# Kernel optimization log

Measured on AMD Instinct MI355X. Metric: run time of the kernel, lower is better.

The kernel has to match this reference:

```python
import jax, jax.numpy as jnp
import numpy as np
import math

H = 768
NH = 12
D = H // NH


def setup_inputs() -> dict:
    key = jax.random.key(0)
    ks = jax.random.split(key, 13)
    B, S = 1, 384
    s = 0.02
    inp = {
        "hidden_states": jax.random.normal(ks[0], (B, S, H), jnp.float32),
        "attention_mask": jnp.zeros((B, 1, 1, S), jnp.float32),
        "pos_emb": jax.random.normal(ks[1], (B, S, S, H), jnp.float32),
        "Wq": jax.random.normal(ks[2], (H, H), jnp.float32) * s,
        "bq": jnp.zeros((H,), jnp.float32),
        "Wk": jax.random.normal(ks[3], (H, H), jnp.float32) * s,
        "bk": jnp.zeros((H,), jnp.float32),
        "Wv": jax.random.normal(ks[4], (H, H), jnp.float32) * s,
        "bv": jnp.zeros((H,), jnp.float32),
        "Wpk": jax.random.normal(ks[5], (H, H), jnp.float32) * s,
        "bpk": jnp.zeros((H,), jnp.float32),
        "Wpq": jax.random.normal(ks[6], (H, H), jnp.float32) * s,
        "bpq": jnp.zeros((H,), jnp.float32),
    }
    return inp


def reference(hidden_states, attention_mask, pos_emb,
              Wq, bq, Wk, bk, Wv, bv, Wpk, bpk, Wpq, bpq):
    B, S, Hd = hidden_states.shape
    split = lambda x: x.reshape(B, S, NH, D).transpose(0, 2, 1, 3)  # -> (B, h, S, d)
    q = split(hidden_states @ Wq + bq)
    k = split(hidden_states @ Wk + bk)
    v = split(hidden_states @ Wv + bv)

    # content-to-content
    c2c = jnp.einsum('bhid,bhjd->bhij', q, k)

    # per-pair position projections: (B,S,S,H) -> (B,S,S,h,d)
    pos_key = (pos_emb @ Wpk + bpk).reshape(B, S, S, NH, D)
    pos_query = (pos_emb @ Wpq + bpq).reshape(B, S, S, NH, D)

    # content-to-position: q[b,h,i,:] . pos_key[b,i,j,h,:]
    c2p = jnp.einsum('bhid,bijhd->bhij', q, pos_key)
    # position-to-content: pos_query[b,j,i,h,:] . k[b,h,j,:]
    p2c = jnp.einsum('bjihd,bhjd->bhij', pos_query, k)

    scores = (c2c + c2p + p2c) / math.sqrt(D) + attention_mask
    probs = jax.nn.softmax(scores, axis=-1)  # dropout is identity (p=0 / eval)
    ctx = jnp.einsum('bhij,bhjd->bhid', probs, v)
    return ctx.transpose(0, 2, 1, 3).reshape(B, S, Hd)
```

## Files before the change

### kernel.cpp

```cpp
#include <hip/hip_runtime.h>
#include <math.h>

#define SEQ 384
#define HDIM 768
#define NHEAD 12
#define DHEAD 64

__global__ __launch_bounds__(256)
void qkv_gemm(const float* __restrict__ X,
              const float* __restrict__ Wq, const float* __restrict__ bq,
              const float* __restrict__ Wk, const float* __restrict__ bk,
              const float* __restrict__ Wv, const float* __restrict__ bv,
              float* __restrict__ q, float* __restrict__ k, float* __restrict__ v)
{
    __shared__ float Xs[16][68];
    __shared__ float Ws[16][68];
    const int z = blockIdx.z;
    const float* W    = (z == 0) ? Wq : (z == 1) ? Wk : Wv;
    const float* bias = (z == 0) ? bq : (z == 1) ? bk : bv;
    float* out        = (z == 0) ? q  : (z == 1) ? k  : v;

    const int m0 = blockIdx.x * 64;
    const int n0 = blockIdx.y * 64;
    const int tid = threadIdx.x;
    const int ty = tid / 16, tx = tid % 16;

    const int lxm = tid / 4,  lxk = (tid % 4) * 4;
    const int lwk = tid / 16, lwn = (tid % 16) * 4;

    float acc[4][4] = {};

    for (int k0 = 0; k0 < HDIM; k0 += 16) {
        float4 xa = *(const float4*)&X[(m0 + lxm) * HDIM + k0 + lxk];
        float4 wa = *(const float4*)&W[(size_t)(k0 + lwk) * HDIM + n0 + lwn];
        __syncthreads();
        Xs[lxk + 0][lxm] = xa.x; Xs[lxk + 1][lxm] = xa.y;
        Xs[lxk + 2][lxm] = xa.z; Xs[lxk + 3][lxm] = xa.w;
        *(float4*)&Ws[lwk][lwn] = wa;
        __syncthreads();
        #pragma unroll
        for (int kk = 0; kk < 16; kk++) {
            float4 a4 = *(const float4*)&Xs[kk][4 * ty];
            float4 b4 = *(const float4*)&Ws[kk][4 * tx];
            float a[4] = {a4.x, a4.y, a4.z, a4.w};
            float b[4] = {b4.x, b4.y, b4.z, b4.w};
            #pragma unroll
            for (int ia = 0; ia < 4; ia++)
                #pragma unroll
                for (int ib = 0; ib < 4; ib++)
                    acc[ia][ib] = fmaf(a[ia], b[ib], acc[ia][ib]);
        }
    }
    float4 bv4 = *(const float4*)&bias[n0 + 4 * tx];
    #pragma unroll
    for (int ia = 0; ia < 4; ia++) {
        float4 o;
        o.x = acc[ia][0] + bv4.x; o.y = acc[ia][1] + bv4.y;
        o.z = acc[ia][2] + bv4.z; o.w = acc[ia][3] + bv4.w;
        *(float4*)&out[(size_t)(m0 + 4 * ty + ia) * HDIM + n0 + 4 * tx] = o;
    }
}

__global__ __launch_bounds__(256)
void pos_proj(const float* __restrict__ q, const float* __restrict__ k,
              const float* __restrict__ Wpk, const float* __restrict__ Wpq,
              float* __restrict__ qp, float* __restrict__ kp)
{
    __shared__ float As[64][68];
    __shared__ float Bs[64][68];
    const int h = blockIdx.z % NHEAD;
    const int s = blockIdx.z / NHEAD;
    const float* Asrc = s ? k   : q;
    const float* Wsrc = s ? Wpq : Wpk;
    float* out        = s ? kp  : qp;

    const int i0 = blockIdx.x * 64, e0 = blockIdx.y * 64;
    const int tid = threadIdx.x;
    const int dg = tid % 16, row = tid / 16;

    #pragma unroll
    for (int r = 0; r < 4; r++) {
        const int rr = r * 16 + row;
        float4 a4 = *(const float4*)&Asrc[(size_t)(i0 + rr) * HDIM + h * 64 + dg * 4];
        float4 b4 = *(const float4*)&Wsrc[(size_t)(e0 + rr) * HDIM + h * 64 + dg * 4];
        As[dg * 4 + 0][rr - 0] = a4.x; As[dg * 4 + 1][rr] = a4.y;
        As[dg * 4 + 2][rr] = a4.z;     As[dg * 4 + 3][rr] = a4.w;
        Bs[dg * 4 + 0][rr] = b4.x;     Bs[dg * 4 + 1][rr] = b4.y;
        Bs[dg * 4 + 2][rr] = b4.z;     Bs[dg * 4 + 3][rr] = b4.w;
    }
    __syncthreads();

    const int ty = tid / 16, tx = tid % 16;
    float acc[4][4] = {};
    #pragma unroll 4
    for (int d = 0; d < 64; d++) {
        float4 a4 = *(const float4*)&As[d][4 * ty];
        float4 b4 = *(const float4*)&Bs[d][4 * tx];
        float a[4] = {a4.x, a4.y, a4.z, a4.w};
        float b[4] = {b4.x, b4.y, b4.z, b4.w};
        #pragma unroll
        for (int ia = 0; ia < 4; ia++)
            #pragma unroll
            for (int ib = 0; ib < 4; ib++)
                acc[ia][ib] = fmaf(a[ia], b[ib], acc[ia][ib]);
    }
    #pragma unroll
    for (int ia = 0; ia < 4; ia++) {
        float4 o = make_float4(acc[ia][0], acc[ia][1], acc[ia][2], acc[ia][3]);
        *(float4*)&out[((size_t)(i0 + 4 * ty + ia) * NHEAD + h) * HDIM + e0 + 4 * tx] = o;
    }
}

__global__ __launch_bounds__(192)
void scores_pos(const float* __restrict__ pe, const float* __restrict__ qp,
                const float* __restrict__ kp,
                float* __restrict__ A1, float* __restrict__ P2T)
{
    __shared__ float Ps[32][388];
    __shared__ float Ws[32][24];
    const int i  = blockIdx.x;
    const int tid = threadIdx.x;
    const int rg = tid / 96;
    const int jl = tid % 96;

    const float* pebase = pe + (size_t)i * SEQ * HDIM;
    const int wr  = tid / 8;
    const int wec = tid % 8;
    const float* wsrc = (wr < NHEAD)
        ? (qp + ((size_t)i * NHEAD + wr) * HDIM)
        : (kp + ((size_t)i * NHEAD + (wr - NHEAD)) * HDIM);

    float acc[12][4] = {};

    for (int c = 0; c < 24; c++) {
        const int e0 = c * 32;
        __syncthreads();
        float4 w4 = *(const float4*)&wsrc[e0 + wec * 4];
        Ws[wec * 4 + 0][wr] = w4.x; Ws[wec * 4 + 1][wr] = w4.y;
        Ws[wec * 4 + 2][wr] = w4.z; Ws[wec * 4 + 3][wr] = w4.w;
        #pragma unroll
        for (int rnd = 0; rnd < 16; rnd++) {
            const int jrow = rnd * 24 + wr;
            float4 p4 = *(const float4*)&pebase[(size_t)jrow * HDIM + e0 + wec * 4];
            Ps[wec * 4 + 0][jrow] = p4.x; Ps[wec * 4 + 1][jrow] = p4.y;
            Ps[wec * 4 + 2][jrow] = p4.z; Ps[wec * 4 + 3][jrow] = p4.w;
        }
        __syncthreads();
        #pragma unroll 2
        for (int ee = 0; ee < 32; ee++) {
            float4 p4 = *(const float4*)&Ps[ee][4 * jl];
            float4 wa = *(const float4*)&Ws[ee][12 * rg + 0];
            float4 wb = *(const float4*)&Ws[ee][12 * rg + 4];
            float4 wc = *(const float4*)&Ws[ee][12 * rg + 8];
            float p[4] = {p4.x, p4.y, p4.z, p4.w};
            float w[12] = {wa.x, wa.y, wa.z, wa.w, wb.x, wb.y, wb.z, wb.w,
                           wc.x, wc.y, wc.z, wc.w};
            #pragma unroll
            for (int r = 0; r < 12; r++)
                #pragma unroll
                for (int u = 0; u < 4; u++)
                    acc[r][u] = fmaf(w[r], p[u], acc[r][u]);
        }
    }
    float* dst = (rg == 0) ? A1 : P2T;
    #pragma unroll
    for (int r = 0; r < 12; r++) {
        float4 o = make_float4(acc[r][0], acc[r][1], acc[r][2], acc[r][3]);
        *(float4*)&dst[((size_t)r * SEQ + i) * SEQ + 4 * jl] = o;
    }
}

__global__ __launch_bounds__(384)
void attn_out(const float* __restrict__ A1, const float* __restrict__ P2T,
              const float* __restrict__ q, const float* __restrict__ k,
              const float* __restrict__ v,
              const float* __restrict__ bpk, const float* __restrict__ bpq,
              const float* __restrict__ mask, float* __restrict__ out)
{
    const int i = blockIdx.x, h = blockIdx.y;
    const int tid = threadIdx.x;
    __shared__ float q_s[64], bk_s[64], bq_s[64];
    __shared__ float p_s[SEQ];
    __shared__ float redm[6], reds[6], redv[6 * 64];

    if (tid < 64)       q_s[tid]        = q[(size_t)i * HDIM + h * 64 + tid];
    else if (tid < 128) bk_s[tid - 64]  = bpk[h * 64 + tid - 64];
    else if (tid < 192) bq_s[tid - 128] = bpq[h * 64 + tid - 128];
    __syncthreads();

    const float* kr = k + (size_t)tid * HDIM + h * 64;
    float c2c = 0.f, kb = 0.f;
    #pragma unroll
    for (int dd = 0; dd < 16; dd++) {
        float4 k4 = *(const float4*)(kr + 4 * dd);
        c2c = fmaf(q_s[4 * dd + 0], k4.x, c2c);
        c2c = fmaf(q_s[4 * dd + 1], k4.y, c2c);
        c2c = fmaf(q_s[4 * dd + 2], k4.z, c2c);
        c2c = fmaf(q_s[4 * dd + 3], k4.w, c2c);
        kb  = fmaf(bq_s[4 * dd + 0], k4.x, kb);
        kb  = fmaf(bq_s[4 * dd + 1], k4.y, kb);
        kb  = fmaf(bq_s[4 * dd + 2], k4.z, kb);
        kb  = fmaf(bq_s[4 * dd + 3], k4.w, kb);
    }
    float qb = 0.f;
    #pragma unroll 8
    for (int d = 0; d < 64; d++) qb = fmaf(q_s[d], bk_s[d], qb);

    float sc = (A1[((size_t)h * SEQ + i) * SEQ + tid] +
                P2T[((size_t)h * SEQ + tid) * SEQ + i] +
                c2c + kb + qb) * 0.125f + mask[tid];

    const int lane = tid & 63, w = tid >> 6;
    float m = sc;
    #pragma unroll
    for (int o = 32; o; o >>= 1) m = fmaxf(m, __shfl_xor(m, o));
    if (lane == 0) redm[w] = m;
    __syncthreads();
    m = redm[0];
    #pragma unroll
    for (int t = 1; t < 6; t++) m = fmaxf(m, redm[t]);

    float p = __expf(sc - m);
    float sum = p;
    #pragma unroll
    for (int o = 32; o; o >>= 1) sum += __shfl_xor(sum, o);
    if (lane == 0) reds[w] = sum;
    p_s[tid] = p;
    __syncthreads();
    const float SUM = reds[0] + reds[1] + reds[2] + reds[3] + reds[4] + reds[5];

    float accv = 0.f;
    const float* vbase = v + h * 64 + lane;
    const int j0 = w * 64;
    #pragma unroll 8
    for (int jj = 0; jj < 64; jj++)
        accv = fmaf(p_s[j0 + jj], vbase[(size_t)(j0 + jj) * HDIM], accv);
    redv[w * 64 + lane] = accv;
    __syncthreads();
    if (tid < 64) {
        float o = redv[tid] + redv[64 + tid] + redv[128 + tid] +
                  redv[192 + tid] + redv[256 + tid] + redv[320 + tid];
        out[(size_t)i * HDIM + h * 64 + tid] = o / SUM;
    }
}

extern "C" void kernel_launch(void* const* d_in, const int* in_sizes, int n_in,
                              void* d_out, int out_size, void* d_ws, size_t ws_size,
                              hipStream_t stream)
{
    const float* hs   = (const float*)d_in[0];
    const float* mask = (const float*)d_in[1];
    const float* pe   = (const float*)d_in[2];
    const float* Wq   = (const float*)d_in[3];
    const float* bq   = (const float*)d_in[4];
    const float* Wk   = (const float*)d_in[5];
    const float* bk   = (const float*)d_in[6];
    const float* Wv   = (const float*)d_in[7];
    const float* bv   = (const float*)d_in[8];
    const float* Wpk  = (const float*)d_in[9];
    const float* bpk  = (const float*)d_in[10];
    const float* Wpq  = (const float*)d_in[11];
    const float* bpq  = (const float*)d_in[12];

    float* ws = (float*)d_ws;
    const size_t SZ_QKV = (size_t)SEQ * HDIM;
    const size_t SZ_QP  = (size_t)SEQ * NHEAD * HDIM;
    const size_t SZ_SC  = (size_t)NHEAD * SEQ * SEQ;
    float* q   = ws;
    float* k   = q  + SZ_QKV;
    float* v   = k  + SZ_QKV;
    float* qp  = v  + SZ_QKV;
    float* kp  = qp + SZ_QP;
    float* A1  = kp + SZ_QP;
    float* P2T = A1 + SZ_SC;

    qkv_gemm<<<dim3(6, 12, 3), 256, 0, stream>>>(hs, Wq, bq, Wk, bk, Wv, bv, q, k, v);
    pos_proj<<<dim3(6, 12, 24), 256, 0, stream>>>(q, k, Wpk, Wpq, qp, kp);
    scores_pos<<<dim3(SEQ), 192, 0, stream>>>(pe, qp, kp, A1, P2T);
    attn_out<<<dim3(SEQ, NHEAD), 384, 0, stream>>>(A1, P2T, q, k, v, bpk, bpq, mask,
                                                   (float*)d_out);
}
```

Before: 861.3 us.

## Restructure scores_pos with 4 waves, split-K over e, and scalar weight loads

The scores_pos kernel now runs 256 threads as four waves. Each wave pair handles one of the qp/kp groups, and the two waves in a pair split the 32-wide e chunk in half. The weights are read with wave-uniform addresses straight from global memory instead of being staged in LDS, and each lane covers 6 j columns. The two partial sums are reduced through LDS at the end, followed by coalesced float4 stores. The aim is better occupancy and less LDS traffic in the dominant pos_emb-streaming kernel, at the cost of an extra reduction and more registers.

```diff
diff --git a/kernel.cpp b/kernel.cpp
--- a/kernel.cpp
+++ b/kernel.cpp
@@ -83,10 +83,10 @@
         const int rr = r * 16 + row;
         float4 a4 = *(const float4*)&Asrc[(size_t)(i0 + rr) * HDIM + h * 64 + dg * 4];
         float4 b4 = *(const float4*)&Wsrc[(size_t)(e0 + rr) * HDIM + h * 64 + dg * 4];
-        As[dg * 4 + 0][rr - 0] = a4.x; As[dg * 4 + 1][rr] = a4.y;
-        As[dg * 4 + 2][rr] = a4.z;     As[dg * 4 + 3][rr] = a4.w;
-        Bs[dg * 4 + 0][rr] = b4.x;     Bs[dg * 4 + 1][rr] = b4.y;
-        Bs[dg * 4 + 2][rr] = b4.z;     Bs[dg * 4 + 3][rr] = b4.w;
+        As[dg * 4 + 0][rr] = a4.x; As[dg * 4 + 1][rr] = a4.y;
+        As[dg * 4 + 2][rr] = a4.z; As[dg * 4 + 3][rr] = a4.w;
+        Bs[dg * 4 + 0][rr] = b4.x; Bs[dg * 4 + 1][rr] = b4.y;
+        Bs[dg * 4 + 2][rr] = b4.z; Bs[dg * 4 + 3][rr] = b4.w;
     }
     __syncthreads();
 
@@ -111,62 +111,94 @@
     }
 }
 
-__global__ __launch_bounds__(192)
+__global__ __launch_bounds__(256)
 void scores_pos(const float* __restrict__ pe, const float* __restrict__ qp,
                 const float* __restrict__ kp,
                 float* __restrict__ A1, float* __restrict__ P2T)
 {
-    __shared__ float Ps[32][388];
-    __shared__ float Ws[32][24];
-    const int i  = blockIdx.x;
-    const int tid = threadIdx.x;
-    const int rg = tid / 96;
-    const int jl = tid % 96;
+    __shared__ float lds[32 * 388];
+    const int i    = blockIdx.x;
+    const int tid  = threadIdx.x;
+    const int lane = tid & 63;
+    const int wave = tid >> 6;
+    const int rgu = __builtin_amdgcn_readfirstlane(wave >> 1);
+    const int esu = __builtin_amdgcn_readfirstlane(wave & 1);
 
     const float* pebase = pe + (size_t)i * SEQ * HDIM;
-    const int wr  = tid / 8;
-    const int wec = tid % 8;
-    const float* wsrc = (wr < NHEAD)
-        ? (qp + ((size_t)i * NHEAD + wr) * HDIM)
-        : (kp + ((size_t)i * NHEAD + (wr - NHEAD)) * HDIM);
-
-    float acc[12][4] = {};
+    const float* wb = (rgu ? kp : qp) + (size_t)i * NHEAD * HDIM;
+
+    const int wr  = tid >> 3;
+    const int wec = tid & 7;
+
+    float acc[12][6] = {};
 
     for (int c = 0; c < 24; c++) {
         const int e0 = c * 32;
         __syncthreads();
-        float4 w4 = *(const float4*)&wsrc[e0 + wec * 4];
-        Ws[wec * 4 + 0][wr] = w4.x; Ws[wec * 4 + 1][wr] = w4.y;
-        Ws[wec * 4 + 2][wr] = w4.z; Ws[wec * 4 + 3][wr] = w4.w;
-        #pragma unroll
-        for (int rnd = 0; rnd < 16; rnd++) {
-            const int jrow = rnd * 24 + wr;
-            float4 p4 = *(const float4*)&pebase[(size_t)jrow * HDIM + e0 + wec * 4];
-            Ps[wec * 4 + 0][jrow] = p4.x; Ps[wec * 4 + 1][jrow] = p4.y;
-            Ps[wec * 4 + 2][jrow] = p4.z; Ps[wec * 4 + 3][jrow] = p4.w;
+        #pragma unroll
+        for (int rnd = 0; rnd < 6; rnd++) {
+            const int jb = rnd * 64 + wr * 2;
+            float4 g0 = *(const float4*)&pebase[(size_t)jb * HDIM + e0 + wec * 4];
+            float4 g1 = *(const float4*)&pebase[(size_t)(jb + 1) * HDIM + e0 + wec * 4];
+            *(float2*)&lds[(wec * 4 + 0) * 388 + jb] = make_float2(g0.x, g1.x);
+            *(float2*)&lds[(wec * 4 + 1) * 388 + jb] = make_float2(g0.y, g1.y);
+            *(float2*)&lds[(wec * 4 + 2) * 388 + jb] = make_float2(g0.z, g1.z);
+            *(float2*)&lds[(wec * 4 + 3) * 388 + jb] = make_float2(g0.w, g1.w);
         }
         __syncthreads();
-        #pragma unroll 2
-        for (int ee = 0; ee < 32; ee++) {
-            float4 p4 = *(const float4*)&Ps[ee][4 * jl];
-            float4 wa = *(const float4*)&Ws[ee][12 * rg + 0];
-            float4 wb = *(const float4*)&Ws[ee][12 * rg + 4];
-            float4 wc = *(const float4*)&Ws[ee][12 * rg + 8];
-            float p[4] = {p4.x, p4.y, p4.z, p4.w};
-            float w[12] = {wa.x, wa.y, wa.z, wa.w, wb.x, wb.y, wb.z, wb.w,
-                           wc.x, wc.y, wc.z, wc.w};
+        const float* wc = wb + e0 + esu * 16;
+        #pragma unroll 4
+        for (int ee = 0; ee < 16; ee++) {
+            const int ei = esu * 16 + ee;
+            float4 p4 = *(const float4*)&lds[ei * 388 + lane * 4];
+            float2 p2 = *(const float2*)&lds[ei * 388 + 256 + lane * 2];
             #pragma unroll
-            for (int r = 0; r < 12; r++)
-                #pragma unroll
-                for (int u = 0; u < 4; u++)
-                    acc[r][u] = fmaf(w[r], p[u], acc[r][u]);
-        }
-    }
-    float* dst = (rg == 0) ? A1 : P2T;
-    #pragma unroll
-    for (int r = 0; r < 12; r++) {
-        float4 o = make_float4(acc[r][0], acc[r][1], acc[r][2], acc[r][3]);
-        *(float4*)&dst[((size_t)r * SEQ + i) * SEQ + 4 * jl] = o;
+            for (int r = 0; r < 12; r++) {
+                const float w = wc[r * HDIM + ee];
+                acc[r][0] = fmaf(w, p4.x, acc[r][0]);
+                acc[r][1] = fmaf(w, p4.y, acc[r][1]);
+                acc[r][2] = fmaf(w, p4.z, acc[r][2]);
+                acc[r][3] = fmaf(w, p4.w, acc[r][3]);
+                acc[r][4] = fmaf(w, p2.x, acc[r][4]);
+                acc[r][5] = fmaf(w, p2.y, acc[r][5]);
+            }
+        }
+    }
+
+    __syncthreads();
+    if (esu == 1) {
+        #pragma unroll
+        for (int r = 0; r < 12; r++) {
+            const int row = rgu * 12 + r;
+            *(float4*)&lds[row * 392 + lane * 4] =
+                make_float4(acc[r][0], acc[r][1], acc[r][2], acc[r][3]);
+            *(float2*)&lds[row * 392 + 256 + lane * 2] =
+                make_float2(acc[r][4], acc[r][5]);
+        }
+    }
+    __syncthreads();
+    if (esu == 0) {
+        #pragma unroll
+        for (int r = 0; r < 12; r++) {
+            const int row = rgu * 12 + r;
+            float4 o4 = *(const float4*)&lds[row * 392 + lane * 4];
+            float2 o2 = *(const float2*)&lds[row * 392 + 256 + lane * 2];
+            o4.x += acc[r][0]; o4.y += acc[r][1]; o4.z += acc[r][2]; o4.w += acc[r][3];
+            o2.x += acc[r][4]; o2.y += acc[r][5];
+            *(float4*)&lds[row * 392 + lane * 4] = o4;
+            *(float2*)&lds[row * 392 + 256 + lane * 2] = o2;
+        }
+    }
+    __syncthreads();
+
+    for (int t = tid; t < 24 * 96; t += 256) {
+        const int row = t / 96;
+        const int c4  = (t % 96) * 4;
+        float4 o = *(const float4*)&lds[row * 392 + c4];
+        float* dst = (row < 12)
+            ? &A1[((size_t)row * SEQ + i) * SEQ + c4]
+            : &P2T[((size_t)(row - 12) * SEQ + i) * SEQ + c4];
+        *(float4*)dst = o;
     }
 }
 
@@ -276,7 +308,7 @@
 
     qkv_gemm<<<dim3(6, 12, 3), 256, 0, stream>>>(hs, Wq, bq, Wk, bk, Wv, bv, q, k, v);
     pos_proj<<<dim3(6, 12, 24), 256, 0, stream>>>(q, k, Wpk, Wpq, qp, kp);
-    scores_pos<<<dim3(SEQ), 192, 0, stream>>>(pe, qp, kp, A1, P2T);
+    scores_pos<<<dim3(SEQ), 256, 0, stream>>>(pe, qp, kp, A1, P2T);
     attn_out<<<dim3(SEQ, NHEAD), 384, 0, stream>>>(A1, P2T, q, k, v, bpk, bpq, mask,
                                                    (float*)d_out);
 }
```

New measurement: 858.2 us. About the same (-0.4%).
